# Optimization experiments

Measured on AMD Instinct MI355X. Metric: run time of the kernel, lower is better.

Reference implementation:

```python
import jax, jax.numpy as jnp
import numpy as np

N = 100000
E = 1600000
CIN = 32
COUT = 32
K = 5
EPS = 1e-15      # PyG GMMConv EPS in sigma^2 denominator
BN_EPS = 1e-5    # torch BatchNorm1d default eps


def gmm_conv(x, edge_index, edge_attr, g, mu, sigma, root, bias):
    """PyG GMMConv (MoNet), aggr='mean', root_weight=True, bias=True."""
    src, dst = edge_index[0], edge_index[1]
    n = x.shape[0]
    k = mu.shape[0]
    cout = root.shape[1]
    xg = (x @ g).reshape(n, k, cout)                # [N, K, out]
    xj = xg[src]                                    # gather: [E, K, out]
    d = edge_attr[:, None, :] - mu[None, :, :]      # [E, K, 3]
    w = jnp.exp(-0.5 * jnp.sum(d * d / (EPS + sigma[None] ** 2), axis=-1))  # [E, K]
    msg = jnp.einsum('eko,ek->eo', xj, w)           # [E, out]
    agg = jax.ops.segment_sum(msg, dst, num_segments=n)
    cnt = jax.ops.segment_sum(jnp.ones((msg.shape[0],), x.dtype), dst, num_segments=n)
    agg = agg / jnp.clip(cnt, 1.0)[:, None]         # mean aggregation
    return agg + x @ root + bias


def batch_norm(x, gamma, beta):
    # training-mode BatchNorm1d: biased batch statistics over node dim
    m = x.mean(0)
    v = x.var(0)
    return (x - m) * jax.lax.rsqrt(v + BN_EPS) * gamma + beta


def setup_inputs() -> dict:
    key = jax.random.key(0)
    ks = jax.random.split(key, 12)
    p = lambda k, s, sc=0.1: jax.random.normal(k, s, jnp.float32) * sc
    return {
        'x': jax.random.normal(ks[0], (N, CIN), jnp.float32),
        'edge_index': jax.random.randint(ks[1], (2, E), 0, N, jnp.int32),
        'edge_attr': jax.random.uniform(ks[2], (E, 3), jnp.float32),
        # left conv1: in -> out, K=5
        'g1': p(ks[3], (CIN, K * COUT)), 'mu1': p(ks[4], (K, 3), 1.0), 'sigma1': jnp.ones((K, 3), jnp.float32),
        'root1': p(ks[5], (CIN, COUT)), 'b1': jnp.zeros((COUT,), jnp.float32),
        'gam1': jnp.ones((COUT,), jnp.float32), 'bet1': jnp.zeros((COUT,), jnp.float32),
        # left conv2: out -> out, K=5
        'g2': p(ks[6], (COUT, K * COUT)), 'mu2': p(ks[7], (K, 3), 1.0), 'sigma2': jnp.ones((K, 3), jnp.float32),
        'root2': p(ks[8], (COUT, COUT)), 'b2': jnp.zeros((COUT,), jnp.float32),
        'gam2': jnp.ones((COUT,), jnp.float32), 'bet2': jnp.zeros((COUT,), jnp.float32),
        # shortcut conv: in -> out, K=1
        'gs': p(ks[9], (CIN, 1 * COUT)), 'mus': p(ks[10], (1, 3), 1.0), 'sigmas': jnp.ones((1, 3), jnp.float32),
        'roots': p(ks[11], (CIN, COUT)), 'bs': jnp.zeros((COUT,), jnp.float32),
        'gams': jnp.ones((COUT,), jnp.float32), 'bets': jnp.zeros((COUT,), jnp.float32),
    }


def reference(x, edge_index, edge_attr,
              g1, mu1, sigma1, root1, b1, gam1, bet1,
              g2, mu2, sigma2, root2, b2, gam2, bet2,
              gs, mus, sigmas, roots, bs, gams, bets):
    h = jax.nn.elu(batch_norm(gmm_conv(x, edge_index, edge_attr, g1, mu1, sigma1, root1, b1), gam1, bet1))
    h = batch_norm(gmm_conv(h, edge_index, edge_attr, g2, mu2, sigma2, root2, b2), gam2, bet2)
    s = batch_norm(gmm_conv(x, edge_index, edge_attr, gs, mus, sigmas, roots, bs), gams, bets)
    return jax.nn.elu(h + s)
```

## Files before the change

kernel.cpp:

```cpp
#include <hip/hip_runtime.h>
#include <hip/hip_bf16.h>
#include <math.h>


#define ELU(v) ((v) > 0.f ? (v) : (__expf(v) - 1.f))

using short8  = __attribute__((ext_vector_type(8))) short;
using floatx4 = __attribute__((ext_vector_type(4))) float;

__device__ inline ushort f2bf(float f) {
    __hip_bfloat16 h = __float2bfloat16(f);
    return *reinterpret_cast<ushort*>(&h);
}
__device__ inline float bflo(unsigned u) { return __uint_as_float(u << 16); }
__device__ inline float bfhi(unsigned u) { return __uint_as_float(u & 0xffff0000u); }
__device__ inline unsigned pack_bf2(float lo, float hi) {
    return ((unsigned)f2bf(hi) << 16) | (unsigned)f2bf(lo);
}

__global__ __launch_bounds__(256) void prep_a(
    const float* __restrict__ x, unsigned* __restrict__ AGGb, int N)
{
    const int idx = blockIdx.x * blockDim.x + threadIdx.x;
    if (idx >= N * 16) return;
    const int n = idx >> 4, l = idx & 15;
    const float2 p = ((const float2*)x)[idx];
    AGGb[(size_t)n * 112 + 96 + l] = pack_bf2(p.x, p.y);
}

__global__ __launch_bounds__(256) void prep_b(
    const float* __restrict__ out1, const float* __restrict__ coef,
    unsigned* __restrict__ AGGb, int N)
{
    const int idx = blockIdx.x * blockDim.x + threadIdx.x;
    if (idx >= N * 16) return;
    const int n = idx >> 4, l = idx & 15;
    const float2 p = ((const float2*)out1)[idx];
    const int c0 = 2 * l, c1 = 2 * l + 1;
    float v0 = p.x * coef[c0] + coef[32 + c0];
    float v1 = p.y * coef[c1] + coef[32 + c1];
    v0 = ELU(v0); v1 = ELU(v1);
    AGGb[(size_t)n * 96 + 80 + l] = pack_bf2(v0, v1);
}

#define CH 4096
__global__ __launch_bounds__(256) void binfill_k(
    const int* __restrict__ ei, const float* __restrict__ attr,
    int* __restrict__ gcur, unsigned long long* __restrict__ pay0,
    int E, int NB, int CAPc)
{
    __shared__ unsigned long long srec[CH];
    __shared__ unsigned char sbin[CH];
    __shared__ int cnt[256], offs[256], wcur[256], gbase[256], sc[256];

    const int t = threadIdx.x;
    const int e0 = blockIdx.x * CH;
    const int nrec = min(CH, E - e0);

    cnt[t] = 0;
    __syncthreads();

    unsigned long long rec[16];
    int bin[16];
#pragma unroll
    for (int r = 0; r < 16; ++r) {
        const int e = e0 + r * 256 + t;
        bin[r] = -1;
        if (e < E) {
            const int s = ei[e], d = ei[E + e];
            const float a0 = attr[(size_t)e * 3 + 0];
            const float a1 = attr[(size_t)e * 3 + 1];
            const float a2 = attr[(size_t)e * 3 + 2];
            const unsigned q0 = (unsigned)min(max((int)(a0 * 4096.f), 0), 4095);
            const unsigned q1 = (unsigned)min(max((int)(a1 * 4096.f), 0), 4095);
            const unsigned q2 = (unsigned)min(max((int)(a2 * 4096.f), 0), 4095);
            rec[r] = (unsigned long long)(unsigned)s
                   | ((unsigned long long)(d & 511) << 17)
                   | ((unsigned long long)q0 << 26)
                   | ((unsigned long long)q1 << 38)
                   | ((unsigned long long)q2 << 50);
            bin[r] = d >> 9;
            atomicAdd(&cnt[bin[r]], 1);
        }
    }
    __syncthreads();

    const int v = cnt[t];
    sc[t] = v;
    __syncthreads();
    for (int o = 1; o < 256; o <<= 1) {
        const int xx = (t >= o) ? sc[t - o] : 0;
        __syncthreads();
        sc[t] += xx;
        __syncthreads();
    }
    offs[t] = sc[t] - v;
    wcur[t] = sc[t] - v;
    __syncthreads();

#pragma unroll
    for (int r = 0; r < 16; ++r) {
        if (bin[r] >= 0) {
            const int pos = atomicAdd(&wcur[bin[r]], 1);
            srec[pos] = rec[r];
            sbin[pos] = (unsigned char)bin[r];
        }
    }
    __syncthreads();

    if (t < NB && cnt[t] > 0) gbase[t] = atomicAdd(&gcur[t], cnt[t]);
    __syncthreads();

    for (int i = t; i < nrec; i += 256) {
        const int b = sbin[i];
        const int idx = gbase[b] + (i - offs[b]);
        if (idx < CAPc)
            pay0[(size_t)b * CAPc + idx] = srec[i];
    }
}

__global__ void bucket_scan(const int* __restrict__ gcur, int* __restrict__ bbase,
                            int NB)
{
    __shared__ int sh[256];
    const int t = threadIdx.x;
    const int v = (t < NB) ? gcur[t] : 0;
    sh[t] = v;
    __syncthreads();
    for (int o = 1; o < 256; o <<= 1) {
        const int xx = (t >= o) ? sh[t - o] : 0;
        __syncthreads();
        sh[t] += xx;
        __syncthreads();
    }
    if (t < NB) bbase[t] = sh[t] - v;
}

__global__ __launch_bounds__(256) void scatter2_k(
    const unsigned long long* __restrict__ pay0, const int* __restrict__ gcur,
    const int* __restrict__ bbase, int* __restrict__ row_ptr,
    unsigned long long* __restrict__ pay, int N, int CAPc, int NB)
{
    const int b = blockIdx.x;
    const int t = threadIdx.x;
    const int d0 = b << 9;
    const int nd = min(512, N - d0);

    __shared__ int cnt[512];
    __shared__ int offs[512];
    __shared__ int sscan[256];

    for (int i = t; i < 512; i += 256) cnt[i] = 0;
    __syncthreads();

    const int total = min(gcur[b], CAPc);
    const unsigned long long* src = pay0 + (size_t)b * CAPc;

    for (int i = t; i < total; i += 256) {
        const int dlo = (int)((src[i] >> 17) & 511);
        atomicAdd(&cnt[dlo], 1);
    }
    __syncthreads();

    const int c0 = cnt[2 * t], c1 = cnt[2 * t + 1];
    const int pairsum = c0 + c1;
    sscan[t] = pairsum;
    __syncthreads();
    for (int o = 1; o < 256; o <<= 1) {
        const int xx = (t >= o) ? sscan[t - o] : 0;
        __syncthreads();
        sscan[t] += xx;
        __syncthreads();
    }
    const int excl = sscan[t] - pairsum;
    offs[2 * t] = excl;
    offs[2 * t + 1] = excl + c0;
    __syncthreads();
    const int btotal = sscan[255];

    const int base = bbase[b];
    for (int i = t; i < nd; i += 256) row_ptr[d0 + i] = base + offs[i];
    if (b == NB - 1 && t == 0) row_ptr[N] = base + btotal;

    for (int i = t; i < 512; i += 256) cnt[i] = offs[i];
    __syncthreads();

    for (int i = t; i < total; i += 256) {
        const unsigned long long rec = src[i];
        const int dlo = (int)((rec >> 17) & 511);
        const int p = atomicAdd(&cnt[dlo], 1);
        pay[base + p] = rec;
    }
}

template <int SLS, bool HAS_S>
__global__ __launch_bounds__(256) void gather_k(
    const unsigned* __restrict__ XB,
    const unsigned long long* __restrict__ payload,
    const int* __restrict__ row_ptr,
    const float* __restrict__ mu_m, const float* __restrict__ sg_m,
    const float* __restrict__ mu_s, const float* __restrict__ sg_s,
    unsigned* __restrict__ AGGb,
    int N, int ntiles)
{
    constexpr int KS = HAS_S ? 6 : 5;
    constexpr float DQ = 1.0f / 4096.0f;

    float mm[15], im[15];
#pragma unroll
    for (int i = 0; i < 15; ++i) {
        mm[i] = mu_m[i];
        float s = sg_m[i];
        im[i] = 1.0f / (1e-15f + s * s);
    }
    float ms[3], is[3];
    if (HAS_S) {
#pragma unroll
        for (int i = 0; i < 3; ++i) {
            ms[i] = mu_s[i];
            float s = sg_s[i];
            is[i] = 1.0f / (1e-15f + s * s);
        }
    }

    const int l = threadIdx.x & 15;
    const int g = threadIdx.x >> 4;
    __shared__ float wbuf[16][17][8];

    for (int tile = blockIdx.x; tile < ntiles; tile += gridDim.x) {
        const int dst = tile * 16 + g;
        float2 acc[KS];
#pragma unroll
        for (int k = 0; k < KS; ++k) acc[k] = make_float2(0.f, 0.f);

        int rp0 = 0, deg = 0;
        if (dst < N) { rp0 = row_ptr[dst]; deg = row_ptr[dst + 1] - rp0; }

        auto body = [&](int j) {
            const float4 a = *(const float4*)&wbuf[g][j][0];
            const float4 b = *(const float4*)&wbuf[g][j][4];
            const int sj = __float_as_int(a.x);
            const unsigned u = XB[(size_t)sj * 16 + l];
            const float x0 = bflo(u), x1 = bfhi(u);
            acc[0].x = fmaf(a.y, x0, acc[0].x); acc[0].y = fmaf(a.y, x1, acc[0].y);
            acc[1].x = fmaf(a.z, x0, acc[1].x); acc[1].y = fmaf(a.z, x1, acc[1].y);
            acc[2].x = fmaf(a.w, x0, acc[2].x); acc[2].y = fmaf(a.w, x1, acc[2].y);
            acc[3].x = fmaf(b.x, x0, acc[3].x); acc[3].y = fmaf(b.x, x1, acc[3].y);
            acc[4].x = fmaf(b.y, x0, acc[4].x); acc[4].y = fmaf(b.y, x1, acc[4].y);
            if (HAS_S) {
                acc[5].x = fmaf(b.z, x0, acc[5].x); acc[5].y = fmaf(b.z, x1, acc[5].y);
            }
        };

        for (int base = 0; base < deg; base += 16) {
            const int nj = min(16, deg - base);
            if (l < nj) {
                unsigned long long pq = payload[rp0 + base + l];
                const int src = (int)(pq & 0x1FFFFull);
                float p0 = ((int)((pq >> 26) & 0xFFF) + 0.5f) * DQ;
                float p1 = ((int)((pq >> 38) & 0xFFF) + 0.5f) * DQ;
                float p2 = ((int)((pq >> 50) & 0xFFF) + 0.5f) * DQ;
                float w[5], wS = 0.f;
#pragma unroll
                for (int k = 0; k < 5; ++k) {
                    float d0 = p0 - mm[k * 3 + 0];
                    float d1 = p1 - mm[k * 3 + 1];
                    float d2 = p2 - mm[k * 3 + 2];
                    float q = d0 * d0 * im[k * 3 + 0] + d1 * d1 * im[k * 3 + 1]
                            + d2 * d2 * im[k * 3 + 2];
                    w[k] = __expf(-0.5f * q);
                }
                if (HAS_S) {
                    float d0 = p0 - ms[0], d1 = p1 - ms[1], d2 = p2 - ms[2];
                    float q = d0 * d0 * is[0] + d1 * d1 * is[1] + d2 * d2 * is[2];
                    wS = __expf(-0.5f * q);
                }
                float4* wp = (float4*)&wbuf[g][l][0];
                wp[0] = make_float4(__int_as_float(src), w[0], w[1], w[2]);
                wp[1] = make_float4(w[3], w[4], wS, 0.f);
            }
            int j = 0;
            for (; j + 3 < nj; j += 4) { body(j); body(j + 1); body(j + 2); body(j + 3); }
            for (; j < nj; ++j) body(j);
        }

        if (dst < N) {
            const float invd = 1.0f / fmaxf((float)deg, 1.0f);
            unsigned* out = AGGb + (size_t)dst * (SLS * 16) + l;
#pragma unroll
            for (int k = 0; k < KS; ++k)
                out[k * 16] = pack_bf2(acc[k].x * invd, acc[k].y * invd);
        }
    }
}

template <bool HAS_S>
__global__ __launch_bounds__(256) void transform_k(
    const unsigned* __restrict__ AGGb,
    const float* __restrict__ g,
    const float* __restrict__ rootm,
    const float* __restrict__ bm,
    const float* __restrict__ gss,
    const float* __restrict__ rootss,
    const float* __restrict__ bss,
    float* __restrict__ out_m, float* __restrict__ out_s,
    float* __restrict__ stats_m, float* __restrict__ stats_s,
    int N)
{
    constexpr int SLS = HAS_S ? 7 : 6;
    const int lane = threadIdx.x & 63;
    const int l4 = lane & 15, quad = lane >> 4;
    const int wv = threadIdx.x >> 6;

    short8 Bc[6][2];
#pragma unroll
    for (int s = 0; s < 5; ++s)
#pragma unroll
        for (int t = 0; t < 2; ++t)
#pragma unroll
            for (int j = 0; j < 8; ++j)
                Bc[s][t][j] = (short)f2bf(g[(quad * 8 + j) * 160 + s * 32 + 16 * t + l4]);
#pragma unroll
    for (int t = 0; t < 2; ++t)
#pragma unroll
        for (int j = 0; j < 8; ++j)
            Bc[5][t][j] = (short)f2bf(rootm[(quad * 8 + j) * 32 + 16 * t + l4]);

    short8 Bs2[2][2];
    if (HAS_S) {
#pragma unroll
        for (int t = 0; t < 2; ++t)
#pragma unroll
            for (int j = 0; j < 8; ++j) {
                Bs2[0][t][j] = (short)f2bf(gss[(quad * 8 + j) * 32 + 16 * t + l4]);
                Bs2[1][t][j] = (short)f2bf(rootss[(quad * 8 + j) * 32 + 16 * t + l4]);
            }
    }

    const float bm0 = bm[l4], bm1 = bm[16 + l4];
    const float bs0 = HAS_S ? bss[l4] : 0.f;
    const float bs1 = HAS_S ? bss[16 + l4] : 0.f;

    const int ngroups = (N + 15) >> 4;
    float ps0 = 0, pq0 = 0, ps1 = 0, pq1 = 0;
    float psS0 = 0, pqS0 = 0, psS1 = 0, pqS1 = 0;

    for (int grp = blockIdx.x * 4 + wv; grp < ngroups; grp += gridDim.x * 4) {
        const int node0 = grp * 16;
        const int myn = min(node0 + l4, N - 1);
        const unsigned* arow = AGGb + (size_t)myn * (SLS * 16) + quad * 4;

        floatx4 acc0 = {0.f, 0.f, 0.f, 0.f}, acc1 = {0.f, 0.f, 0.f, 0.f};
#pragma unroll
        for (int s = 0; s < 6; ++s) {
            const int slot = (s < 5) ? s : (SLS - 1);
            const uint4 av = *(const uint4*)(arow + 16 * slot);
            const short8 A = *reinterpret_cast<const short8*>(&av);
            acc0 = __builtin_amdgcn_mfma_f32_16x16x32_bf16(A, Bc[s][0], acc0, 0, 0, 0);
            acc1 = __builtin_amdgcn_mfma_f32_16x16x32_bf16(A, Bc[s][1], acc1, 0, 0, 0);
        }
        floatx4 accS0 = {0.f, 0.f, 0.f, 0.f}, accS1 = {0.f, 0.f, 0.f, 0.f};
        if (HAS_S) {
#pragma unroll
            for (int s = 0; s < 2; ++s) {
                const int slot = 5 + s;
                const uint4 av = *(const uint4*)(arow + 16 * slot);
                const short8 A = *reinterpret_cast<const short8*>(&av);
                accS0 = __builtin_amdgcn_mfma_f32_16x16x32_bf16(A, Bs2[s][0], accS0, 0, 0, 0);
                accS1 = __builtin_amdgcn_mfma_f32_16x16x32_bf16(A, Bs2[s][1], accS1, 0, 0, 0);
            }
        }

#pragma unroll
        for (int r = 0; r < 4; ++r) {
            const int n = node0 + quad * 4 + r;
            if (n < N) {
                float v0 = acc0[r] + bm0;
                float v1 = acc1[r] + bm1;
                out_m[(size_t)n * 32 + l4] = v0;
                out_m[(size_t)n * 32 + 16 + l4] = v1;
                ps0 += v0; pq0 += v0 * v0;
                ps1 += v1; pq1 += v1 * v1;
                if (HAS_S) {
                    float s0 = accS0[r] + bs0;
                    float s1 = accS1[r] + bs1;
                    out_s[(size_t)n * 32 + l4] = s0;
                    out_s[(size_t)n * 32 + 16 + l4] = s1;
                    psS0 += s0; pqS0 += s0 * s0;
                    psS1 += s1; pqS1 += s1 * s1;
                }
            }
        }
    }

    __shared__ float sred[64];
    const int tid = threadIdx.x;
    const int spread = (blockIdx.x & 7) * 64;
    {
        if (tid < 64) sred[tid] = 0.f;
        __syncthreads();
        atomicAdd(&sred[l4], ps0);       atomicAdd(&sred[16 + l4], ps1);
        atomicAdd(&sred[32 + l4], pq0);  atomicAdd(&sred[48 + l4], pq1);
        __syncthreads();
        if (tid < 64) atomicAdd(&stats_m[spread + tid], sred[tid]);
        __syncthreads();
    }
    if (HAS_S) {
        if (tid < 64) sred[tid] = 0.f;
        __syncthreads();
        atomicAdd(&sred[l4], psS0);      atomicAdd(&sred[16 + l4], psS1);
        atomicAdd(&sred[32 + l4], pqS0); atomicAdd(&sred[48 + l4], pqS1);
        __syncthreads();
        if (tid < 64) atomicAdd(&stats_s[spread + tid], sred[tid]);
    }
}

__global__ void coef_k(const float* __restrict__ stats, const float* __restrict__ gam,
                       const float* __restrict__ bet, float* __restrict__ coef,
                       float invN)
{
    int c = threadIdx.x;
    if (c < 32) {
        float s = 0.f, q = 0.f;
        for (int p = 0; p < 8; ++p) { s += stats[p * 64 + c]; q += stats[p * 64 + 32 + c]; }
        float m = s * invN;
        float v = fmaxf(q * invN - m * m, 0.f);
        float sc = gam[c] * rsqrtf(v + 1e-5f);
        coef[c] = sc;
        coef[32 + c] = bet[c] - m * sc;
    }
}

__global__ __launch_bounds__(256) void final_k(
    const float* __restrict__ o2, const float* __restrict__ os,
    const float* __restrict__ c2, const float* __restrict__ cs,
    float* __restrict__ out, int total)
{
    int idx = blockIdx.x * blockDim.x + threadIdx.x;
    if (idx >= total) return;
    int c = idx & 31;
    float v = o2[idx] * c2[c] + c2[32 + c] + os[idx] * cs[c] + cs[32 + c];
    out[idx] = ELU(v);
}

extern "C" void kernel_launch(void* const* d_in, const int* in_sizes, int n_in,
                              void* d_out, int out_size, void* d_ws, size_t ws_size,
                              hipStream_t stream)
{
    const float* x      = (const float*)d_in[0];
    const int*   ei     = (const int*)d_in[1];
    const float* attr   = (const float*)d_in[2];
    const float* g1     = (const float*)d_in[3];
    const float* mu1    = (const float*)d_in[4];
    const float* sig1   = (const float*)d_in[5];
    const float* root1  = (const float*)d_in[6];
    const float* b1     = (const float*)d_in[7];
    const float* gam1   = (const float*)d_in[8];
    const float* bet1   = (const float*)d_in[9];
    const float* g2     = (const float*)d_in[10];
    const float* mu2    = (const float*)d_in[11];
    const float* sig2   = (const float*)d_in[12];
    const float* root2  = (const float*)d_in[13];
    const float* b2     = (const float*)d_in[14];
    const float* gam2   = (const float*)d_in[15];
    const float* bet2   = (const float*)d_in[16];
    const float* gs     = (const float*)d_in[17];
    const float* mus    = (const float*)d_in[18];
    const float* sigs   = (const float*)d_in[19];
    const float* roots  = (const float*)d_in[20];
    const float* bs     = (const float*)d_in[21];
    const float* gams   = (const float*)d_in[22];
    const float* bets   = (const float*)d_in[23];

    const int N = in_sizes[0] / 32;
    const int E = in_sizes[1] / 2;
    const int total = N * 32;
    const int ntiles = (N + 15) / 16;
    const int NB = (N + 511) >> 9;
    const int CAPc = ((((E + NB - 1) / NB) * 5) / 4 + 15) & ~15;

    char* ws = (char*)d_ws;
    size_t off = 0;
    auto carve = [&](size_t bytes) {
        void* p = ws + off;
        off = (off + bytes + 255) & ~(size_t)255;
        return p;
    };
    unsigned* XB   = (unsigned*)carve((size_t)N * 16 * 4);
    unsigned* AGGb = (unsigned*)carve((size_t)N * 112 * 4);
    float*  OUT1   = (float*)carve((size_t)N * 32 * 4);
    float*  OUT2   = (float*)carve((size_t)N * 32 * 4);
    float*  OUTS   = (float*)carve((size_t)N * 32 * 4);
    unsigned long long* PAY  = (unsigned long long*)carve((size_t)E * 8);
    unsigned long long* PAY0 = (unsigned long long*)carve((size_t)NB * CAPc * 8);
    int*    ROWP   = (int*)carve((size_t)(N + 1) * 4);
    int*    GCUR   = (int*)carve(512 * 4);
    int*    BBASE  = GCUR + 256;
    float*  STATS  = (float*)carve(3 * 512 * 4);
    float*  COEF   = (float*)carve(3 * 64 * 4);
    float* stats1 = STATS, *stats2 = STATS + 512, *statsS = STATS + 1024;
    float* coef1 = COEF, *coef2 = COEF + 64, *coefS = COEF + 128;
    (void)ws_size; (void)n_in; (void)out_size;

    const float invN = 1.0f / (float)N;
    const int ew = (total + 255) / 256;
    const int epb = (N * 16 + 255) / 256;
    const int nfb = (E + CH - 1) / CH;

    hipMemsetAsync(GCUR, 0, 256 * 4, stream);
    hipMemsetAsync(STATS, 0, 3 * 512 * 4, stream);

    binfill_k<<<nfb, 256, 0, stream>>>(ei, attr, GCUR, PAY0, E, NB, CAPc);
    bucket_scan<<<1, 256, 0, stream>>>(GCUR, BBASE, NB);
    scatter2_k<<<NB, 256, 0, stream>>>(PAY0, GCUR, BBASE, ROWP, PAY, N, CAPc, NB);

    prep_a<<<epb, 256, 0, stream>>>(x, AGGb, N);
    {
    }
    extern __global__ void prep_xb(const float*, unsigned*, int);
    prep_xb<<<epb, 256, 0, stream>>>(x, XB, N);

    gather_k<7, true><<<ntiles, 256, 0, stream>>>(XB, PAY, ROWP,
        mu1, sig1, mus, sigs, AGGb, N, ntiles);
    transform_k<true><<<1024, 256, 0, stream>>>(AGGb, g1, root1, b1,
        gs, roots, bs, OUT1, OUTS, stats1, statsS, N);
    coef_k<<<1, 64, 0, stream>>>(stats1, gam1, bet1, coef1, invN);
    coef_k<<<1, 64, 0, stream>>>(statsS, gams, bets, coefS, invN);

    prep_b<<<epb, 256, 0, stream>>>(OUT1, coef1, AGGb, N);
    extern __global__ void prep_hxb(const float*, const float*, unsigned*, int);
    prep_hxb<<<epb, 256, 0, stream>>>(OUT1, coef1, XB, N);
    gather_k<6, false><<<ntiles, 256, 0, stream>>>(XB, PAY, ROWP,
        mu2, sig2, nullptr, nullptr, AGGb, N, ntiles);
    transform_k<false><<<1024, 256, 0, stream>>>(AGGb, g2, root2, b2,
        nullptr, nullptr, nullptr, OUT2, nullptr, stats2, nullptr, N);
    coef_k<<<1, 64, 0, stream>>>(stats2, gam2, bet2, coef2, invN);

    final_k<<<ew, 256, 0, stream>>>(OUT2, OUTS, coef2, coefS, (float*)d_out, total);
}

__global__ __launch_bounds__(256) void prep_xb(
    const float* __restrict__ x, unsigned* __restrict__ XB, int N)
{
    const int idx = blockIdx.x * blockDim.x + threadIdx.x;
    if (idx >= N * 16) return;
    const float2 p = ((const float2*)x)[idx];
    XB[idx] = pack_bf2(p.x, p.y);
}

__global__ __launch_bounds__(256) void prep_hxb(
    const float* __restrict__ out1, const float* __restrict__ coef,
    unsigned* __restrict__ XB, int N)
{
    const int idx = blockIdx.x * blockDim.x + threadIdx.x;
    if (idx >= N * 16) return;
    const int l = idx & 15;
    const float2 p = ((const float2*)out1)[idx];
    const int c0 = 2 * l, c1 = 2 * l + 1;
    float v0 = p.x * coef[c0] + coef[32 + c0];
    float v1 = p.y * coef[c1] + coef[32 + c1];
    v0 = ELU(v0); v1 = ELU(v1);
    XB[idx] = pack_bf2(v0, v1);
}
```

Before: 326.5 us.

## Fold prep kernels into binfill/transform, fuse bucket scan into scatter, merge coef launches

Several launch-reducing changes land together. The x-to-bf16 conversion moves into binfill_k, and prep_a/prep_b are removed, so the transform reads its root operand directly from XB instead of a copied AGGb slot. The bucket prefix scan is folded into scatter2_k, which now runs 512 threads per block and does a per-block reduction over gcur. The two coef kernels are merged and the two memsets are combined into one. The binfill chunk is halved and gather accumulation uses packed float2 FMA, trading fewer launches and less AGGb traffic for more binfill blocks and redundant reductions.

```diff
diff --git a/kernel.cpp b/kernel.cpp
--- a/kernel.cpp
+++ b/kernel.cpp
@@ -7,6 +7,7 @@
 
 using short8  = __attribute__((ext_vector_type(8))) short;
 using floatx4 = __attribute__((ext_vector_type(4))) float;
+using v2f     = __attribute__((ext_vector_type(2))) float;
 
 __device__ inline ushort f2bf(float f) {
     __hip_bfloat16 h = __float2bfloat16(f);
@@ -18,35 +19,26 @@
     return ((unsigned)f2bf(hi) << 16) | (unsigned)f2bf(lo);
 }
 
-__global__ __launch_bounds__(256) void prep_a(
-    const float* __restrict__ x, unsigned* __restrict__ AGGb, int N)
+__global__ __launch_bounds__(256) void prep_hxb(
+    const float* __restrict__ out1, const float* __restrict__ coef,
+    unsigned* __restrict__ XB, int N)
 {
     const int idx = blockIdx.x * blockDim.x + threadIdx.x;
     if (idx >= N * 16) return;
-    const int n = idx >> 4, l = idx & 15;
-    const float2 p = ((const float2*)x)[idx];
-    AGGb[(size_t)n * 112 + 96 + l] = pack_bf2(p.x, p.y);
-}
-
-__global__ __launch_bounds__(256) void prep_b(
-    const float* __restrict__ out1, const float* __restrict__ coef,
-    unsigned* __restrict__ AGGb, int N)
-{
-    const int idx = blockIdx.x * blockDim.x + threadIdx.x;
-    if (idx >= N * 16) return;
-    const int n = idx >> 4, l = idx & 15;
+    const int l = idx & 15;
     const float2 p = ((const float2*)out1)[idx];
     const int c0 = 2 * l, c1 = 2 * l + 1;
     float v0 = p.x * coef[c0] + coef[32 + c0];
     float v1 = p.y * coef[c1] + coef[32 + c1];
     v0 = ELU(v0); v1 = ELU(v1);
-    AGGb[(size_t)n * 96 + 80 + l] = pack_bf2(v0, v1);
-}
-
-#define CH 4096
+    XB[idx] = pack_bf2(v0, v1);
+}
+
+#define CH 2048
 __global__ __launch_bounds__(256) void binfill_k(
     const int* __restrict__ ei, const float* __restrict__ attr,
     int* __restrict__ gcur, unsigned long long* __restrict__ pay0,
+    const float* __restrict__ x, unsigned* __restrict__ XB, int nxb,
     int E, int NB, int CAPc)
 {
     __shared__ unsigned long long srec[CH];
@@ -57,13 +49,21 @@
     const int e0 = blockIdx.x * CH;
     const int nrec = min(CH, E - e0);
 
+    for (int i = t; i < CH; i += 256) {
+        const int idx = e0 + i;
+        if (idx < nxb) {
+            const float2 p = ((const float2*)x)[idx];
+            XB[idx] = pack_bf2(p.x, p.y);
+        }
+    }
+
     cnt[t] = 0;
     __syncthreads();
 
-    unsigned long long rec[16];
-    int bin[16];
-#pragma unroll
-    for (int r = 0; r < 16; ++r) {
+    unsigned long long rec[8];
+    int bin[8];
+#pragma unroll
+    for (int r = 0; r < 8; ++r) {
         const int e = e0 + r * 256 + t;
         bin[r] = -1;
         if (e < E) {
@@ -99,7 +99,7 @@
     __syncthreads();
 
 #pragma unroll
-    for (int r = 0; r < 16; ++r) {
+    for (int r = 0; r < 8; ++r) {
         if (bin[r] >= 0) {
             const int pos = atomicAdd(&wcur[bin[r]], 1);
             srec[pos] = rec[r];
@@ -119,27 +119,10 @@
     }
 }
 
-__global__ void bucket_scan(const int* __restrict__ gcur, int* __restrict__ bbase,
-                            int NB)
-{
-    __shared__ int sh[256];
-    const int t = threadIdx.x;
-    const int v = (t < NB) ? gcur[t] : 0;
-    sh[t] = v;
-    __syncthreads();
-    for (int o = 1; o < 256; o <<= 1) {
-        const int xx = (t >= o) ? sh[t - o] : 0;
-        __syncthreads();
-        sh[t] += xx;
-        __syncthreads();
-    }
-    if (t < NB) bbase[t] = sh[t] - v;
-}
-
-__global__ __launch_bounds__(256) void scatter2_k(
+__global__ __launch_bounds__(512) void scatter2_k(
     const unsigned long long* __restrict__ pay0, const int* __restrict__ gcur,
-    const int* __restrict__ bbase, int* __restrict__ row_ptr,
-    unsigned long long* __restrict__ pay, int N, int CAPc, int NB)
+    int* __restrict__ row_ptr, unsigned long long* __restrict__ pay,
+    int N, int CAPc, int NB)
 {
     const int b = blockIdx.x;
     const int t = threadIdx.x;
@@ -148,44 +131,47 @@
 
     __shared__ int cnt[512];
     __shared__ int offs[512];
-    __shared__ int sscan[256];
-
-    for (int i = t; i < 512; i += 256) cnt[i] = 0;
-    __syncthreads();
+    __shared__ int sscan[512];
+    __shared__ int ssum[512];
+
+    ssum[t] = (t < b && t < NB) ? gcur[t] : 0;
+    cnt[t] = 0;
+    __syncthreads();
+    for (int o = 256; o > 0; o >>= 1) {
+        if (t < o) ssum[t] += ssum[t + o];
+        __syncthreads();
+    }
+    const int base = ssum[0];
 
     const int total = min(gcur[b], CAPc);
     const unsigned long long* src = pay0 + (size_t)b * CAPc;
 
-    for (int i = t; i < total; i += 256) {
+    for (int i = t; i < total; i += 512) {
         const int dlo = (int)((src[i] >> 17) & 511);
         atomicAdd(&cnt[dlo], 1);
     }
     __syncthreads();
 
-    const int c0 = cnt[2 * t], c1 = cnt[2 * t + 1];
-    const int pairsum = c0 + c1;
-    sscan[t] = pairsum;
-    __syncthreads();
-    for (int o = 1; o < 256; o <<= 1) {
+    const int v = cnt[t];
+    sscan[t] = v;
+    __syncthreads();
+    for (int o = 1; o < 512; o <<= 1) {
         const int xx = (t >= o) ? sscan[t - o] : 0;
         __syncthreads();
         sscan[t] += xx;
         __syncthreads();
     }
-    const int excl = sscan[t] - pairsum;
-    offs[2 * t] = excl;
-    offs[2 * t + 1] = excl + c0;
-    __syncthreads();
-    const int btotal = sscan[255];
-
-    const int base = bbase[b];
-    for (int i = t; i < nd; i += 256) row_ptr[d0 + i] = base + offs[i];
+    offs[t] = sscan[t] - v;
+    __syncthreads();
+    const int btotal = sscan[511];
+
+    if (t < nd) row_ptr[d0 + t] = base + offs[t];
     if (b == NB - 1 && t == 0) row_ptr[N] = base + btotal;
 
-    for (int i = t; i < 512; i += 256) cnt[i] = offs[i];
-    __syncthreads();
-
-    for (int i = t; i < total; i += 256) {
+    cnt[t] = offs[t];
+    __syncthreads();
+
+    for (int i = t; i < total; i += 512) {
         const unsigned long long rec = src[i];
         const int dlo = (int)((rec >> 17) & 511);
         const int p = atomicAdd(&cnt[dlo], 1);
@@ -193,7 +179,7 @@
     }
 }
 
-template <int SLS, bool HAS_S>
+template <bool HAS_S>
 __global__ __launch_bounds__(256) void gather_k(
     const unsigned* __restrict__ XB,
     const unsigned long long* __restrict__ payload,
@@ -229,9 +215,9 @@
 
     for (int tile = blockIdx.x; tile < ntiles; tile += gridDim.x) {
         const int dst = tile * 16 + g;
-        float2 acc[KS];
-#pragma unroll
-        for (int k = 0; k < KS; ++k) acc[k] = make_float2(0.f, 0.f);
+        v2f acc[KS];
+#pragma unroll
+        for (int k = 0; k < KS; ++k) acc[k] = (v2f){0.f, 0.f};
 
         int rp0 = 0, deg = 0;
         if (dst < N) { rp0 = row_ptr[dst]; deg = row_ptr[dst + 1] - rp0; }
@@ -241,25 +227,24 @@
             const float4 b = *(const float4*)&wbuf[g][j][4];
             const int sj = __float_as_int(a.x);
             const unsigned u = XB[(size_t)sj * 16 + l];
-            const float x0 = bflo(u), x1 = bfhi(u);
-            acc[0].x = fmaf(a.y, x0, acc[0].x); acc[0].y = fmaf(a.y, x1, acc[0].y);
-            acc[1].x = fmaf(a.z, x0, acc[1].x); acc[1].y = fmaf(a.z, x1, acc[1].y);
-            acc[2].x = fmaf(a.w, x0, acc[2].x); acc[2].y = fmaf(a.w, x1, acc[2].y);
-            acc[3].x = fmaf(b.x, x0, acc[3].x); acc[3].y = fmaf(b.x, x1, acc[3].y);
-            acc[4].x = fmaf(b.y, x0, acc[4].x); acc[4].y = fmaf(b.y, x1, acc[4].y);
-            if (HAS_S) {
-                acc[5].x = fmaf(b.z, x0, acc[5].x); acc[5].y = fmaf(b.z, x1, acc[5].y);
-            }
+            const v2f xv = {bflo(u), bfhi(u)};
+            acc[0] = __builtin_elementwise_fma((v2f){a.y, a.y}, xv, acc[0]);
+            acc[1] = __builtin_elementwise_fma((v2f){a.z, a.z}, xv, acc[1]);
+            acc[2] = __builtin_elementwise_fma((v2f){a.w, a.w}, xv, acc[2]);
+            acc[3] = __builtin_elementwise_fma((v2f){b.x, b.x}, xv, acc[3]);
+            acc[4] = __builtin_elementwise_fma((v2f){b.y, b.y}, xv, acc[4]);
+            if (HAS_S)
+                acc[5] = __builtin_elementwise_fma((v2f){b.z, b.z}, xv, acc[5]);
         };
 
         for (int base = 0; base < deg; base += 16) {
             const int nj = min(16, deg - base);
             if (l < nj) {
-                unsigned long long pq = payload[rp0 + base + l];
-                const int src = (int)(pq & 0x1FFFFull);
-                float p0 = ((int)((pq >> 26) & 0xFFF) + 0.5f) * DQ;
-                float p1 = ((int)((pq >> 38) & 0xFFF) + 0.5f) * DQ;
-                float p2 = ((int)((pq >> 50) & 0xFFF) + 0.5f) * DQ;
+                unsigned long long pq8 = payload[rp0 + base + l];
+                const int src = (int)(pq8 & 0x1FFFFull);
+                float p0 = ((int)((pq8 >> 26) & 0xFFF) + 0.5f) * DQ;
+                float p1 = ((int)((pq8 >> 38) & 0xFFF) + 0.5f) * DQ;
+                float p2 = ((int)((pq8 >> 50) & 0xFFF) + 0.5f) * DQ;
                 float w[5], wS = 0.f;
 #pragma unroll
                 for (int k = 0; k < 5; ++k) {
@@ -286,10 +271,10 @@
 
         if (dst < N) {
             const float invd = 1.0f / fmaxf((float)deg, 1.0f);
-            unsigned* out = AGGb + (size_t)dst * (SLS * 16) + l;
+            unsigned* out = AGGb + (size_t)dst * (KS * 16) + l;
 #pragma unroll
             for (int k = 0; k < KS; ++k)
-                out[k * 16] = pack_bf2(acc[k].x * invd, acc[k].y * invd);
+                out[k * 16] = pack_bf2(acc[k][0] * invd, acc[k][1] * invd);
         }
     }
 }
@@ -297,6 +282,7 @@
 template <bool HAS_S>
 __global__ __launch_bounds__(256) void transform_k(
     const unsigned* __restrict__ AGGb,
+    const unsigned* __restrict__ XBd,
     const float* __restrict__ g,
     const float* __restrict__ rootm,
     const float* __restrict__ bm,
@@ -307,7 +293,7 @@
     float* __restrict__ stats_m, float* __restrict__ stats_s,
     int N)
 {
-    constexpr int SLS = HAS_S ? 7 : 6;
+    constexpr int KS = HAS_S ? 6 : 5;
     const int lane = threadIdx.x & 63;
     const int l4 = lane & 15, quad = lane >> 4;
     const int wv = threadIdx.x >> 6;
@@ -348,27 +334,29 @@
     for (int grp = blockIdx.x * 4 + wv; grp < ngroups; grp += gridDim.x * 4) {
         const int node0 = grp * 16;
         const int myn = min(node0 + l4, N - 1);
-        const unsigned* arow = AGGb + (size_t)myn * (SLS * 16) + quad * 4;
+        const unsigned* arow = AGGb + (size_t)myn * (KS * 16) + quad * 4;
+        const uint4 rootA = *(const uint4*)(XBd + (size_t)myn * 16 + quad * 4);
+        const short8 Ar = *reinterpret_cast<const short8*>(&rootA);
 
         floatx4 acc0 = {0.f, 0.f, 0.f, 0.f}, acc1 = {0.f, 0.f, 0.f, 0.f};
 #pragma unroll
-        for (int s = 0; s < 6; ++s) {
-            const int slot = (s < 5) ? s : (SLS - 1);
-            const uint4 av = *(const uint4*)(arow + 16 * slot);
+        for (int s = 0; s < 5; ++s) {
+            const uint4 av = *(const uint4*)(arow + 16 * s);
             const short8 A = *reinterpret_cast<const short8*>(&av);
             acc0 = __builtin_amdgcn_mfma_f32_16x16x32_bf16(A, Bc[s][0], acc0, 0, 0, 0);
             acc1 = __builtin_amdgcn_mfma_f32_16x16x32_bf16(A, Bc[s][1], acc1, 0, 0, 0);
         }
+        acc0 = __builtin_amdgcn_mfma_f32_16x16x32_bf16(Ar, Bc[5][0], acc0, 0, 0, 0);
+        acc1 = __builtin_amdgcn_mfma_f32_16x16x32_bf16(Ar, Bc[5][1], acc1, 0, 0, 0);
+
         floatx4 accS0 = {0.f, 0.f, 0.f, 0.f}, accS1 = {0.f, 0.f, 0.f, 0.f};
         if (HAS_S) {
-#pragma unroll
-            for (int s = 0; s < 2; ++s) {
-                const int slot = 5 + s;
-                const uint4 av = *(const uint4*)(arow + 16 * slot);
-                const short8 A = *reinterpret_cast<const short8*>(&av);
-                accS0 = __builtin_amdgcn_mfma_f32_16x16x32_bf16(A, Bs2[s][0], accS0, 0, 0, 0);
-                accS1 = __builtin_amdgcn_mfma_f32_16x16x32_bf16(A, Bs2[s][1], accS1, 0, 0, 0);
-            }
+            const uint4 av = *(const uint4*)(arow + 16 * 5);
+            const short8 A = *reinterpret_cast<const short8*>(&av);
+            accS0 = __builtin_amdgcn_mfma_f32_16x16x32_bf16(A, Bs2[0][0], accS0, 0, 0, 0);
+            accS1 = __builtin_amdgcn_mfma_f32_16x16x32_bf16(A, Bs2[0][1], accS1, 0, 0, 0);
+            accS0 = __builtin_amdgcn_mfma_f32_16x16x32_bf16(Ar, Bs2[1][0], accS0, 0, 0, 0);
+            accS1 = __builtin_amdgcn_mfma_f32_16x16x32_bf16(Ar, Bs2[1][1], accS1, 0, 0, 0);
         }
 
 #pragma unroll
@@ -415,20 +403,28 @@
     }
 }
 
-__global__ void coef_k(const float* __restrict__ stats, const float* __restrict__ gam,
-                       const float* __restrict__ bet, float* __restrict__ coef,
-                       float invN)
-{
-    int c = threadIdx.x;
-    if (c < 32) {
-        float s = 0.f, q = 0.f;
-        for (int p = 0; p < 8; ++p) { s += stats[p * 64 + c]; q += stats[p * 64 + 32 + c]; }
-        float m = s * invN;
-        float v = fmaxf(q * invN - m * m, 0.f);
-        float sc = gam[c] * rsqrtf(v + 1e-5f);
-        coef[c] = sc;
-        coef[32 + c] = bet[c] - m * sc;
-    }
+__global__ void coef2_k(const float* __restrict__ stats1, const float* __restrict__ gam1,
+                        const float* __restrict__ bet1, float* __restrict__ coef1,
+                        const float* __restrict__ stats2, const float* __restrict__ gam2,
+                        const float* __restrict__ bet2, float* __restrict__ coef2,
+                        float invN)
+{
+    const int t = threadIdx.x;
+    const int set = t >> 6;
+    const int c = t & 63;
+    if (c >= 32) return;
+    const float* stats = set ? stats2 : stats1;
+    const float* gam = set ? gam2 : gam1;
+    const float* bet = set ? bet2 : bet1;
+    float* coef = set ? coef2 : coef1;
+    if (set && !stats) return;
+    float s = 0.f, q = 0.f;
+    for (int p = 0; p < 8; ++p) { s += stats[p * 64 + c]; q += stats[p * 64 + 32 + c]; }
+    float m = s * invN;
+    float v = fmaxf(q * invN - m * m, 0.f);
+    float sc = gam[c] * rsqrtf(v + 1e-5f);
+    coef[c] = sc;
+    coef[32 + c] = bet[c] - m * sc;
 }
 
 __global__ __launch_bounds__(256) void final_k(
@@ -487,15 +483,14 @@
         return p;
     };
     unsigned* XB   = (unsigned*)carve((size_t)N * 16 * 4);
-    unsigned* AGGb = (unsigned*)carve((size_t)N * 112 * 4);
+    unsigned* AGGb = (unsigned*)carve((size_t)N * 96 * 4);
     float*  OUT1   = (float*)carve((size_t)N * 32 * 4);
     float*  OUT2   = (float*)carve((size_t)N * 32 * 4);
     float*  OUTS   = (float*)carve((size_t)N * 32 * 4);
     unsigned long long* PAY  = (unsigned long long*)carve((size_t)E * 8);
     unsigned long long* PAY0 = (unsigned long long*)carve((size_t)NB * CAPc * 8);
     int*    ROWP   = (int*)carve((size_t)(N + 1) * 4);
-    int*    GCUR   = (int*)carve(512 * 4);
-    int*    BBASE  = GCUR + 256;
+    int*    GCUR   = (int*)carve(256 * 4);
     float*  STATS  = (float*)carve(3 * 512 * 4);
     float*  COEF   = (float*)carve(3 * 64 * 4);
     float* stats1 = STATS, *stats2 = STATS + 512, *statsS = STATS + 1024;
@@ -507,58 +502,25 @@
     const int epb = (N * 16 + 255) / 256;
     const int nfb = (E + CH - 1) / CH;
 
-    hipMemsetAsync(GCUR, 0, 256 * 4, stream);
-    hipMemsetAsync(STATS, 0, 3 * 512 * 4, stream);
-
-    binfill_k<<<nfb, 256, 0, stream>>>(ei, attr, GCUR, PAY0, E, NB, CAPc);
-    bucket_scan<<<1, 256, 0, stream>>>(GCUR, BBASE, NB);
-    scatter2_k<<<NB, 256, 0, stream>>>(PAY0, GCUR, BBASE, ROWP, PAY, N, CAPc, NB);
-
-    prep_a<<<epb, 256, 0, stream>>>(x, AGGb, N);
-    {
-    }
-    extern __global__ void prep_xb(const float*, unsigned*, int);
-    prep_xb<<<epb, 256, 0, stream>>>(x, XB, N);
-
-    gather_k<7, true><<<ntiles, 256, 0, stream>>>(XB, PAY, ROWP,
+    hipMemsetAsync(GCUR, 0, 256 * 4 + 3 * 512 * 4, stream);
+
+    binfill_k<<<nfb, 256, 0, stream>>>(ei, attr, GCUR, PAY0, x, XB, N * 16, E, NB, CAPc);
+    scatter2_k<<<NB, 512, 0, stream>>>(PAY0, GCUR, ROWP, PAY, N, CAPc, NB);
+
+    gather_k<true><<<ntiles, 256, 0, stream>>>(XB, PAY, ROWP,
         mu1, sig1, mus, sigs, AGGb, N, ntiles);
-    transform_k<true><<<1024, 256, 0, stream>>>(AGGb, g1, root1, b1,
+    transform_k<true><<<1024, 256, 0, stream>>>(AGGb, XB, g1, root1, b1,
         gs, roots, bs, OUT1, OUTS, stats1, statsS, N);
-    coef_k<<<1, 64, 0, stream>>>(stats1, gam1, bet1, coef1, invN);
-    coef_k<<<1, 64, 0, stream>>>(statsS, gams, bets, coefS, invN);
-
-    prep_b<<<epb, 256, 0, stream>>>(OUT1, coef1, AGGb, N);
-    extern __global__ void prep_hxb(const float*, const float*, unsigned*, int);
+    coef2_k<<<1, 128, 0, stream>>>(stats1, gam1, bet1, coef1,
+                                   statsS, gams, bets, coefS, invN);
+
     prep_hxb<<<epb, 256, 0, stream>>>(OUT1, coef1, XB, N);
-    gather_k<6, false><<<ntiles, 256, 0, stream>>>(XB, PAY, ROWP,
+    gather_k<false><<<ntiles, 256, 0, stream>>>(XB, PAY, ROWP,
         mu2, sig2, nullptr, nullptr, AGGb, N, ntiles);
-    transform_k<false><<<1024, 256, 0, stream>>>(AGGb, g2, root2, b2,
+    transform_k<false><<<1024, 256, 0, stream>>>(AGGb, XB, g2, root2, b2,
         nullptr, nullptr, nullptr, OUT2, nullptr, stats2, nullptr, N);
-    coef_k<<<1, 64, 0, stream>>>(stats2, gam2, bet2, coef2, invN);
+    coef2_k<<<1, 128, 0, stream>>>(stats2, gam2, bet2, coef2,
+                                   nullptr, nullptr, nullptr, nullptr, invN);
 
     final_k<<<ew, 256, 0, stream>>>(OUT2, OUTS, coef2, coefS, (float*)d_out, total);
 }
-
-__global__ __launch_bounds__(256) void prep_xb(
-    const float* __restrict__ x, unsigned* __restrict__ XB, int N)
-{
-    const int idx = blockIdx.x * blockDim.x + threadIdx.x;
-    if (idx >= N * 16) return;
-    const float2 p = ((const float2*)x)[idx];
-    XB[idx] = pack_bf2(p.x, p.y);
-}
-
-__global__ __launch_bounds__(256) void prep_hxb(
-    const float* __restrict__ out1, const float* __restrict__ coef,
-    unsigned* __restrict__ XB, int N)
-{
-    const int idx = blockIdx.x * blockDim.x + threadIdx.x;
-    if (idx >= N * 16) return;
-    const int l = idx & 15;
-    const float2 p = ((const float2*)out1)[idx];
-    const int c0 = 2 * l, c1 = 2 * l + 1;
-    float v0 = p.x * coef[c0] + coef[32 + c0];
-    float v1 = p.y * coef[c1] + coef[32 + c1];
-    v0 = ELU(v0); v1 = ELU(v1);
-    XB[idx] = pack_bf2(v0, v1);
-}
```

Result: no change. 325.1 us (-0.4%).
